# Optimization experiments

Measured on AMD Instinct MI355X. Metric: run time of the kernel, lower is better.

Reference implementation:

```python
import jax, jax.numpy as jnp
import numpy as np

B, T, M, PH, PW = 4, 8, 128, 48, 48
QD, CD, H, DH = 1024, 768, 8, 64
INNER = H * DH

def layer_norm(x, g, b, eps=1e-5):
    m = x.mean(-1, keepdims=True)
    v = ((x - m) ** 2).mean(-1, keepdims=True)
    return (x - m) * jax.lax.rsqrt(v + eps) * g + b

def setup_inputs():
    key = jax.random.key(0)
    ks = jax.random.split(key, 10)
    x = jax.random.normal(ks[0], (B * T, PH * PW, QD), jnp.float32)
    context = jax.random.normal(ks[1], (B, M, CD), jnp.float32)
    sg_node_positions = jax.random.normal(ks[2], (B, M, 3), jnp.float32) * 2.0
    # valid c2w: identity rotation + random translation (invertible)
    c2w = jnp.broadcast_to(jnp.eye(4, dtype=jnp.float32), (B, T, 4, 4))
    camera_c2w = c2w.at[..., :3, 3].set(jax.random.normal(ks[3], (B, T, 3), jnp.float32))
    intrinsics = jnp.broadcast_to(jnp.array([[1.0, 0.0, 0.5], [0.0, 1.0, 0.5], [0.0, 0.0, 1.0]], jnp.float32), (B, 3, 3))
    s = 0.02
    Wq = jax.random.normal(ks[4], (QD, INNER), jnp.float32) * s
    Wk = jax.random.normal(ks[5], (CD, INNER), jnp.float32) * s
    Wv = jax.random.normal(ks[6], (CD, INNER), jnp.float32) * s
    Wo = jax.random.normal(ks[7], (INNER, QD), jnp.float32) * s
    gate = jnp.array([0.1], jnp.float32)          # zero-init in module; nonzero so path is active
    spatial_gate = jnp.array([0.1], jnp.float32)
    spatial_log_sigma = jax.random.normal(ks[8], (H,), jnp.float32) * 0.1
    depth_log_alpha = jax.random.normal(ks[9], (H,), jnp.float32) * 0.1
    gamma_q = jnp.ones((QD,), jnp.float32); beta_q = jnp.zeros((QD,), jnp.float32)
    gamma_k = jnp.ones((CD,), jnp.float32); beta_k = jnp.zeros((CD,), jnp.float32)
    return dict(x=x, context=context, sg_node_positions=sg_node_positions, camera_c2w=camera_c2w,
                intrinsics=intrinsics, Wq=Wq, Wk=Wk, Wv=Wv, Wo=Wo, gate=gate, spatial_gate=spatial_gate,
                spatial_log_sigma=spatial_log_sigma, depth_log_alpha=depth_log_alpha,
                gamma_q=gamma_q, beta_q=beta_q, gamma_k=gamma_k, beta_k=beta_k,
                patch_h=PH, patch_w=PW)

def spatial_bias(sg_node_positions, camera_c2w, intrinsics, spatial_log_sigma, depth_log_alpha, patch_h, patch_w):
    Bb, Mn, _ = sg_node_positions.shape
    Tn = camera_c2w.shape[1]
    w2c = jnp.linalg.inv(camera_c2w)
    R = w2c[:, :, :3, :3]
    tv = w2c[:, :, :3, 3]
    p_cam = jnp.einsum('btij,bmj->btmi', R, sg_node_positions) + tv[:, :, None, :]  # (B,T,M,3)
    z = jnp.clip(p_cam[..., 2], 1e-4, None)
    fx = intrinsics[:, 0, 0]; fy = intrinsics[:, 1, 1]
    cx = intrinsics[:, 0, 2]; cy = intrinsics[:, 1, 2]
    u = fx[:, None, None] * (p_cam[..., 0] / z) + cx[:, None, None]   # (B,T,M)
    v = fy[:, None, None] * (p_cam[..., 1] / z) + cy[:, None, None]
    gy = (jnp.arange(patch_h, dtype=jnp.float32) + 0.5) / patch_h
    gx = (jnp.arange(patch_w, dtype=jnp.float32) + 0.5) / patch_w
    gyy, gxx = jnp.meshgrid(gy, gx, indexing='ij')
    gxx = gxx.reshape(-1); gyy = gyy.reshape(-1)                       # (P,)
    sq = (gxx[None, None, :, None] - u[:, :, None, :]) ** 2 + (gyy[None, None, :, None] - v[:, :, None, :]) ** 2  # (B,T,P,M)
    sigma = jnp.exp(spatial_log_sigma)
    inv2s = z[:, :, None, :] ** 2 / (2.0 * sigma[None, None, :, None] ** 2 + 1e-8)  # (B,T,H,M)
    bias = -sq[:, :, None, :, :] * inv2s[:, :, :, None, :]             # (B,T,H,P,M)
    depth_term = depth_log_alpha[None, None, :, None, None] * (-jnp.log(z))[:, :, None, None, :]
    bias = bias + depth_term
    behind = p_cam[..., 2] <= 0.0
    bias = jnp.where(behind[:, :, None, None, :], 0.0, bias)
    return bias.reshape(Bb * Tn, bias.shape[2], patch_h * patch_w, Mn)  # (BT,H,P,M)

def reference(x, context, sg_node_positions, camera_c2w, intrinsics, Wq, Wk, Wv, Wo, gate, spatial_gate,
              spatial_log_sigma, depth_log_alpha, gamma_q, beta_q, gamma_k, beta_k, patch_h, patch_w):
    BT, P, _ = x.shape
    Bb, Mn, _ = context.shape
    Tn = camera_c2w.shape[1]
    q = layer_norm(x, gamma_q, beta_q) @ Wq                            # (BT,P,INNER)
    ck = layer_norm(context, gamma_k, beta_k)
    k = ck @ Wk
    v = ck @ Wv
    q = q.reshape(BT, P, H, DH).transpose(0, 2, 1, 3)                  # (BT,H,P,DH)
    k = jnp.broadcast_to(k.reshape(Bb, 1, Mn, H, DH), (Bb, Tn, Mn, H, DH)).reshape(BT, Mn, H, DH).transpose(0, 2, 1, 3)
    v = jnp.broadcast_to(v.reshape(Bb, 1, Mn, H, DH), (Bb, Tn, Mn, H, DH)).reshape(BT, Mn, H, DH).transpose(0, 2, 1, 3)
    scores = jnp.einsum('bhpd,bhmd->bhpm', q, k) * (DH ** -0.5)        # (BT,H,P,M)
    bias = spatial_bias(sg_node_positions, camera_c2w, intrinsics, spatial_log_sigma, depth_log_alpha, patch_h, patch_w)
    scores = scores + jnp.tanh(spatial_gate) * bias
    attn = jax.nn.softmax(scores, axis=-1)
    out = jnp.einsum('bhpm,bhmd->bhpd', attn, v).transpose(0, 2, 1, 3).reshape(BT, P, INNER)
    return x + jnp.tanh(gate) * (out @ Wo)
```

## Files before the change

kernel.cpp:

```cpp
#include <hip/hip_runtime.h>
#include <hip/hip_bf16.h>
#include <stdint.h>
#include <cstddef>

typedef short short8 __attribute__((ext_vector_type(8)));
typedef float f32x4 __attribute__((ext_vector_type(4)));
typedef unsigned short us4 __attribute__((ext_vector_type(4)));
typedef unsigned short us8 __attribute__((ext_vector_type(8)));

#define DEV static __device__ __forceinline__

DEV unsigned short f2b(float f) {
  __hip_bfloat16 h = __float2bfloat16(f);
  return __builtin_bit_cast(unsigned short, h);
}

DEV void gload_lds16(const void* g, void* lds) {
  __builtin_amdgcn_global_load_lds((const __attribute__((address_space(1))) unsigned int*)g,
                                   (__attribute__((address_space(3))) unsigned int*)lds, 16, 0, 0);
}

__launch_bounds__(512, 2)
__global__ void gemm256(const unsigned short* __restrict__ A,
                        const unsigned short* __restrict__ Bt,
                        unsigned short* __restrict__ Cb,
                        int M, int N, int K)
{
  __shared__ __attribute__((aligned(16))) char lds[131072];
  const int tid  = threadIdx.x;
  const int lane = tid & 63, w = tid >> 6;
  const int wr = w >> 2, wc = w & 3;
  const int g = lane >> 4, lr = lane & 15;
  const int lrow  = lane >> 3;
  const int lslot = (lane & 7) ^ lrow;

  const int ntile = N >> 8;
  const int nwg = gridDim.x;
  const int bid = blockIdx.x;
  const int tile = ((nwg & 7) == 0) ? ((bid & 7)*(nwg >> 3) + (bid >> 3)) : bid;
  const size_t m0 = (size_t)(tile / ntile) << 8;
  const size_t n0 = (size_t)(tile % ntile) << 8;

  f32x4 acc[8][4] = {};

  auto STAGE = [&](int k0, int bufsel) {
    char* Ad = lds + bufsel*65536 + w*1024;
    char* Bd = Ad + 32768;
#pragma unroll
    for (int j = 0; j < 4; ++j) {
      const int row = j*64 + w*8 + lrow;
      gload_lds16(A  + (m0 + row)*(size_t)K + k0 + lslot*8, Ad + j*8192);
      gload_lds16(Bt + (n0 + row)*(size_t)K + k0 + lslot*8, Bd + j*8192);
    }
  };

  STAGE(0, 0);
  STAGE(64, 1);

  const int NT = K >> 6;
  for (int t = 0; t < NT; ++t) {
    const int cur = t & 1;
    if (t + 1 < NT) { asm volatile("s_waitcnt vmcnt(8)" ::: "memory"); }
    else            { asm volatile("s_waitcnt vmcnt(0)" ::: "memory"); }
    __builtin_amdgcn_s_barrier();
    __builtin_amdgcn_sched_barrier(0);

    const char* Ab = lds + cur*65536;
    const char* Bb = Ab + 32768;
#pragma unroll
    for (int ks = 0; ks < 2; ++ks) {
      short8 bfr[4];
#pragma unroll
      for (int nt = 0; nt < 4; ++nt) {
        const int row = wc*64 + nt*16 + lr;
        const int slot = (ks*4 + g) ^ (row & 7);
        bfr[nt] = *(const short8*)(Bb + row*128 + slot*16);
      }
#pragma unroll
      for (int mt = 0; mt < 8; ++mt) {
        const int row = wr*128 + mt*16 + lr;
        const int slot = (ks*4 + g) ^ (row & 7);
        short8 af = *(const short8*)(Ab + row*128 + slot*16);
#pragma unroll
        for (int nt = 0; nt < 4; ++nt)
          acc[mt][nt] = __builtin_amdgcn_mfma_f32_16x16x32_bf16(af, bfr[nt], acc[mt][nt], 0, 0, 0);
      }
    }

    __builtin_amdgcn_sched_barrier(0);
    __builtin_amdgcn_s_barrier();
    __builtin_amdgcn_sched_barrier(0);
    if (t + 2 < NT) STAGE((t + 2) << 6, cur);
  }

  float* Sw = (float*)(lds) + w*1024;
#pragma unroll
  for (int mt = 0; mt < 8; ++mt) {
#pragma unroll
    for (int nt = 0; nt < 4; ++nt)
#pragma unroll
      for (int r = 0; r < 4; ++r)
        Sw[(g*4 + r)*64 + nt*16 + lr] = acc[mt][nt][r];
#pragma unroll
    for (int rep = 0; rep < 2; ++rep) {
      const int row2 = rep*8 + (lane >> 3);
      const int colf = (lane & 7)*8;
      f32x4 a0 = *(const f32x4*)(Sw + row2*64 + colf);
      f32x4 a1 = *(const f32x4*)(Sw + row2*64 + colf + 4);
      us8 ov;
#pragma unroll
      for (int j = 0; j < 4; ++j) { ov[j] = f2b(a0[j]); ov[4+j] = f2b(a1[j]); }
      const size_t rowg = m0 + wr*128 + mt*16 + row2;
      *(us8*)(Cb + rowg * (size_t)N + (n0 + wc*64 + colf)) = ov;
    }
  }
}

template<int EPI>
__launch_bounds__(256, 2)
__global__ void gemm_bt(const unsigned short* __restrict__ A,
                        const unsigned short* __restrict__ Bt,
                        unsigned short* __restrict__ Cb,
                        float* __restrict__ Cf,
                        const float* __restrict__ xres,
                        const float* __restrict__ gatep,
                        int M, int N, int K)
{
  __shared__ __attribute__((aligned(16))) char As[16384];
  __shared__ __attribute__((aligned(16))) char Bs[16384];
  const int tid  = threadIdx.x;
  const int lane = tid & 63, w = tid >> 6;
  const int wr = w >> 1, wc = w & 1;
  const int g = lane >> 4, lr = lane & 15;
  const int ntile = N >> 7;
  const int nwg = gridDim.x;
  const int bid = blockIdx.x;
  const int tile = ((nwg & 7) == 0) ? ((bid & 7)*(nwg >> 3) + (bid >> 3)) : bid;
  const int m0 = (tile / ntile) << 7;
  const int n0 = (tile % ntile) << 7;

  const int lrow  = lane >> 3;
  const int lslot = (lane & 7) ^ lrow;

  f32x4 acc[4][4] = {};

  for (int k0 = 0; k0 < K; k0 += 64) {
#pragma unroll
    for (int c = 0; c < 4; ++c) {
      const int rowc = (w*4 + c)*8;
      gload_lds16(A  + (size_t)(m0 + rowc + lrow)*K + k0 + lslot*8, As + rowc*128);
      gload_lds16(Bt + (size_t)(n0 + rowc + lrow)*K + k0 + lslot*8, Bs + rowc*128);
    }
    __syncthreads();
#pragma unroll
    for (int ks = 0; ks < 2; ++ks) {
      short8 af[4], bfr[4];
#pragma unroll
      for (int mt = 0; mt < 4; ++mt) {
        int row = wr*64 + mt*16 + lr;
        int slot = (ks*4 + g) ^ (row & 7);
        af[mt] = *(const short8*)(As + row*128 + slot*16);
      }
#pragma unroll
      for (int nt = 0; nt < 4; ++nt) {
        int row = wc*64 + nt*16 + lr;
        int slot = (ks*4 + g) ^ (row & 7);
        bfr[nt] = *(const short8*)(Bs + row*128 + slot*16);
      }
#pragma unroll
      for (int mt = 0; mt < 4; ++mt)
#pragma unroll
        for (int nt = 0; nt < 4; ++nt)
          acc[mt][nt] = __builtin_amdgcn_mfma_f32_16x16x32_bf16(af[mt], bfr[nt], acc[mt][nt], 0, 0, 0);
    }
    __syncthreads();
  }

  float* Sw = (float*)(As) + w*1024;
  if (EPI == 1) {
    const float tg = tanhf(gatep[0]);
#pragma unroll
    for (int mt = 0; mt < 4; ++mt) {
#pragma unroll
      for (int nt = 0; nt < 4; ++nt)
#pragma unroll
        for (int r = 0; r < 4; ++r)
          Sw[(g*4 + r)*64 + nt*16 + lr] = acc[mt][nt][r];
#pragma unroll
      for (int rep = 0; rep < 4; ++rep) {
        int row2 = rep*4 + g;
        int colf = lr*4;
        f32x4 val = *(const f32x4*)(Sw + row2*64 + colf);
        size_t rowg = (size_t)(m0 + wr*64 + mt*16 + row2);
        size_t idx = rowg * (size_t)N + (n0 + wc*64 + colf);
        f32x4 xv = *(const f32x4*)(xres + idx);
#pragma unroll
        for (int j = 0; j < 4; ++j) val[j] = xv[j] + tg*val[j];
        *(f32x4*)(Cf + idx) = val;
      }
    }
  } else {
#pragma unroll
    for (int mt = 0; mt < 4; ++mt) {
#pragma unroll
      for (int nt = 0; nt < 4; ++nt)
#pragma unroll
        for (int r = 0; r < 4; ++r)
          Sw[(g*4 + r)*64 + nt*16 + lr] = acc[mt][nt][r];
#pragma unroll
      for (int rep = 0; rep < 2; ++rep) {
        int row2 = rep*8 + (lane >> 3);
        int colf = (lane & 7)*8;
        f32x4 a0 = *(const f32x4*)(Sw + row2*64 + colf);
        f32x4 a1 = *(const f32x4*)(Sw + row2*64 + colf + 4);
        us8 ov;
#pragma unroll
        for (int j = 0; j < 4; ++j) { ov[j] = f2b(a0[j]); ov[4+j] = f2b(a1[j]); }
        size_t rowg = (size_t)(m0 + wr*64 + mt*16 + row2);
        *(us8*)(Cb + rowg * (size_t)N + (n0 + wc*64 + colf)) = ov;
      }
    }
  }
}

__launch_bounds__(256, 2)
__global__ void gemm_kv(const unsigned short* __restrict__ ck,
                        const unsigned short* __restrict__ Wk_t,
                        const unsigned short* __restrict__ Wv_t,
                        unsigned short* __restrict__ Kb,
                        unsigned short* __restrict__ Vt)
{
  __shared__ __attribute__((aligned(16))) char As[16384];
  __shared__ __attribute__((aligned(16))) char Bs[16384];
  const int bid = blockIdx.x;
  const int kv = bid >> 4, bidl = bid & 15;
  const unsigned short* Bt = kv ? Wv_t : Wk_t;
  const int m0 = (bidl >> 2) << 7, n0 = (bidl & 3) << 7;
  const int tid  = threadIdx.x;
  const int lane = tid & 63, w = tid >> 6;
  const int wr = w >> 1, wc = w & 1;
  const int g = lane >> 4, lr = lane & 15;
  const int lrow  = lane >> 3;
  const int lslot = (lane & 7) ^ lrow;
  const int K = 768;

  f32x4 acc[4][4] = {};

  for (int k0 = 0; k0 < K; k0 += 64) {
#pragma unroll
    for (int c = 0; c < 4; ++c) {
      const int rowc = (w*4 + c)*8;
      gload_lds16(ck + (size_t)(m0 + rowc + lrow)*K + k0 + lslot*8, As + rowc*128);
      gload_lds16(Bt + (size_t)(n0 + rowc + lrow)*K + k0 + lslot*8, Bs + rowc*128);
    }
    __syncthreads();
#pragma unroll
    for (int ks = 0; ks < 2; ++ks) {
      short8 af[4], bfr[4];
#pragma unroll
      for (int mt = 0; mt < 4; ++mt) {
        int row = wr*64 + mt*16 + lr;
        int slot = (ks*4 + g) ^ (row & 7);
        af[mt] = *(const short8*)(As + row*128 + slot*16);
      }
#pragma unroll
      for (int nt = 0; nt < 4; ++nt) {
        int row = wc*64 + nt*16 + lr;
        int slot = (ks*4 + g) ^ (row & 7);
        bfr[nt] = *(const short8*)(Bs + row*128 + slot*16);
      }
#pragma unroll
      for (int mt = 0; mt < 4; ++mt)
#pragma unroll
        for (int nt = 0; nt < 4; ++nt)
          acc[mt][nt] = __builtin_amdgcn_mfma_f32_16x16x32_bf16(af[mt], bfr[nt], acc[mt][nt], 0, 0, 0);
    }
    __syncthreads();
  }

#pragma unroll
  for (int mt = 0; mt < 4; ++mt)
#pragma unroll
    for (int nt = 0; nt < 4; ++nt)
#pragma unroll
      for (int r = 0; r < 4; ++r) {
        int row = m0 + wr*64 + mt*16 + g*4 + r;
        int col = n0 + wc*64 + nt*16 + lr;
        int bb = row >> 7, mm = row & 127, hh = col >> 6, dd = col & 63;
        unsigned short val = f2b(acc[mt][nt][r]);
        if (kv == 0) Kb[(((size_t)(bb*8 + hh))*128 + mm)*64 + dd] = val;
        else         Vt[(((size_t)(bb*8 + hh))*64 + dd)*128 + mm] = val;
      }
}

template<int NSEG>
DEV void ln_rows_body(const float* __restrict__ in, const float* __restrict__ gamma,
                      const float* __restrict__ beta, unsigned short* __restrict__ out,
                      int C, int blk, int tid)
{
  const int lane = tid & 63;
  const size_t row = (size_t)blk*4 + (tid >> 6);
  const float* rp = in + row * (size_t)C;
  f32x4 vals[NSEG];
  float s = 0.f, sq = 0.f;
#pragma unroll
  for (int i = 0; i < NSEG; ++i) {
    f32x4 v = *(const f32x4*)(rp + (i*64 + lane)*4);
    vals[i] = v;
#pragma unroll
    for (int j = 0; j < 4; ++j) { s += v[j]; sq += v[j]*v[j]; }
  }
#pragma unroll
  for (int off = 32; off >= 1; off >>= 1) {
    s  += __shfl_xor(s, off);
    sq += __shfl_xor(sq, off);
  }
  const float invC = 1.0f / (float)C;
  float mean = s * invC;
  float var  = sq * invC - mean*mean;
  float rstd = rsqrtf(var + 1e-5f);
#pragma unroll
  for (int i = 0; i < NSEG; ++i) {
    int cb = (i*64 + lane)*4;
    f32x4 gm = *(const f32x4*)(gamma + cb);
    f32x4 bb = *(const f32x4*)(beta + cb);
    us4 ov;
#pragma unroll
    for (int j = 0; j < 4; ++j)
      ov[j] = f2b((vals[i][j] - mean)*rstd*gm[j] + bb[j]);
    *(us4*)(out + row * (size_t)C + cb) = ov;
  }
}

__global__ void ln_big(const float* __restrict__ in, const float* __restrict__ gamma,
                       const float* __restrict__ beta, unsigned short* __restrict__ out)
{
  ln_rows_body<4>(in, gamma, beta, out, 1024, blockIdx.x, threadIdx.x);
}

__global__ void prep(const float* __restrict__ Wq, const float* __restrict__ Wk,
                     const float* __restrict__ Wv, const float* __restrict__ Wo,
                     unsigned short* __restrict__ Wq_t, unsigned short* __restrict__ Wk_t,
                     unsigned short* __restrict__ Wv_t, unsigned short* __restrict__ Wo_t,
                     const float* __restrict__ ctx, const float* __restrict__ gk,
                     const float* __restrict__ bk, unsigned short* __restrict__ ck,
                     const float* __restrict__ pos, const float* __restrict__ c2w,
                     const float* __restrict__ intr, const float* __restrict__ sls,
                     const float* __restrict__ dla,
                     float* __restrict__ u_o, float* __restrict__ v_o, float* __restrict__ bh_o,
                     float* __restrict__ iv_o, float* __restrict__ dp_o)
{
  __shared__ float tile[32][33];
  int bidx = blockIdx.x;
  if (bidx < 1792) {
    const float* src; unsigned short* dst; int R, C;
    if (bidx < 512)       { src = Wq; dst = Wq_t; R = 1024; C = 512; }
    else if (bidx < 896)  { src = Wk; dst = Wk_t; R = 768;  C = 512;  bidx -= 512; }
    else if (bidx < 1280) { src = Wv; dst = Wv_t; R = 768;  C = 512;  bidx -= 896; }
    else                  { src = Wo; dst = Wo_t; R = 512;  C = 1024; bidx -= 1280; }
    const int cb = C >> 5;
    const int bx = bidx % cb, by = bidx / cb;
    const int tx = threadIdx.x & 31, ty = threadIdx.x >> 5;
#pragma unroll
    for (int i = 0; i < 32; i += 8)
      tile[ty + i][tx] = src[(size_t)(by*32 + ty + i)*C + bx*32 + tx];
    __syncthreads();
#pragma unroll
    for (int i = 0; i < 32; i += 8)
      dst[(size_t)(bx*32 + ty + i)*R + by*32 + tx] = f2b(tile[tx][ty + i]);
    return;
  }
  if (bidx < 1920) {
    ln_rows_body<3>(ctx, gk, bk, ck, 768, bidx - 1792, threadIdx.x);
    return;
  }
  if (threadIdx.x >= 128) return;
  const int bt = bidx - 1920;
  const int b = bt >> 3;
  const int m = threadIdx.x;
  const float* Mc = c2w + (size_t)bt*16;
  float r00=Mc[0], r01=Mc[1], r02=Mc[2],  t0=Mc[3];
  float r10=Mc[4], r11=Mc[5], r12=Mc[6],  t1=Mc[7];
  float r20=Mc[8], r21=Mc[9], r22=Mc[10], t2=Mc[11];
  float a00 = r11*r22 - r12*r21;
  float a01 = r02*r21 - r01*r22;
  float a02 = r01*r12 - r02*r11;
  float a10 = r12*r20 - r10*r22;
  float a11 = r00*r22 - r02*r20;
  float a12 = r02*r10 - r00*r12;
  float a20 = r10*r21 - r11*r20;
  float a21 = r01*r20 - r00*r21;
  float a22 = r00*r11 - r01*r10;
  float det = r00*a00 + r01*a10 + r02*a20;
  float id = 1.0f/det;
  a00*=id; a01*=id; a02*=id; a10*=id; a11*=id; a12*=id; a20*=id; a21*=id; a22*=id;
  float tv0 = -(a00*t0 + a01*t1 + a02*t2);
  float tv1 = -(a10*t0 + a11*t1 + a12*t2);
  float tv2 = -(a20*t0 + a21*t1 + a22*t2);
  const float* pm = pos + (size_t)(b*128 + m)*3;
  float px = pm[0], py = pm[1], pz = pm[2];
  float x = a00*px + a01*py + a02*pz + tv0;
  float y = a10*px + a11*py + a12*pz + tv1;
  float zraw = a20*px + a21*py + a22*pz + tv2;
  float z = fmaxf(zraw, 1e-4f);
  float fx = intr[b*9 + 0], fy = intr[b*9 + 4], cx = intr[b*9 + 2], cy = intr[b*9 + 5];
  u_o[bt*128 + m] = fx*(x/z) + cx;
  v_o[bt*128 + m] = fy*(y/z) + cy;
  bh_o[bt*128 + m] = (zraw <= 0.0f) ? 1.0f : 0.0f;
  float lz = __logf(z);
#pragma unroll
  for (int hh = 0; hh < 8; ++hh) {
    float sg = __expf(sls[hh]);
    iv_o[(size_t)(bt*8 + hh)*128 + m] = z*z / (2.0f*sg*sg + 1e-8f);
    dp_o[(size_t)(bt*8 + hh)*128 + m] = dla[hh] * (-lz);
  }
}

__launch_bounds__(256, 2)
__global__ void attn_kernel(const unsigned short* __restrict__ q,
                            const unsigned short* __restrict__ Kb,
                            const unsigned short* __restrict__ Vt,
                            const float* __restrict__ ub, const float* __restrict__ vb,
                            const float* __restrict__ bhb,
                            const float* __restrict__ ivb, const float* __restrict__ dpb,
                            const float* __restrict__ sgate,
                            unsigned short* __restrict__ out)
{
  const int bid = blockIdx.x;
  const int ptile = bid % 18;
  const int h  = (bid / 18) & 7;
  const int bt = bid / (18*8);
  const int b  = bt >> 3;
  const int lane = threadIdx.x & 63, w = threadIdx.x >> 6;
  const int g = lane >> 4, lr = lane & 15;
  const int p0 = ptile*128 + w*32;

  const float sg = tanhf(sgate[0]);
  const unsigned short* Kh = Kb + ((size_t)(b*8 + h)) * (128*64);
  const unsigned short* Vh = Vt + ((size_t)(b*8 + h)) * (64*128);
  const unsigned short* qh = q + (size_t)bt*2304*512 + h*64;

  short8 qf[2][2];
#pragma unroll
  for (int pt = 0; pt < 2; ++pt)
#pragma unroll
    for (int ks = 0; ks < 2; ++ks)
      qf[pt][ks] = *(const short8*)(qh + (size_t)(p0 + pt*16 + lr)*512 + ks*32 + g*8);

  f32x4 st[8][2] = {};
#pragma unroll
  for (int mt = 0; mt < 8; ++mt) {
#pragma unroll
    for (int ks = 0; ks < 2; ++ks) {
      short8 kf = *(const short8*)(Kh + (mt*16 + lr)*64 + ks*32 + g*8);
#pragma unroll
      for (int pt = 0; pt < 2; ++pt)
        st[mt][pt] = __builtin_amdgcn_mfma_f32_16x16x32_bf16(kf, qf[pt][ks], st[mt][pt], 0, 0, 0);
    }
  }

  float gx[2], gy[2];
#pragma unroll
  for (int pt = 0; pt < 2; ++pt) {
    int p = p0 + pt*16 + lr;
    int py = p / 48, px = p - py*48;
    gx[pt] = (px + 0.5f) * (1.0f/48.0f);
    gy[pt] = (py + 0.5f) * (1.0f/48.0f);
  }
  const float* uB = ub  + bt*128;
  const float* vB = vb  + bt*128;
  const float* bB = bhb + bt*128;
  const float* iB = ivb + (size_t)(bt*8 + h)*128;
  const float* dB = dpb + (size_t)(bt*8 + h)*128;

  float pmax[2] = {-3.0e38f, -3.0e38f};
#pragma unroll
  for (int mt = 0; mt < 8; ++mt) {
    int mb = mt*16 + g*4;
    f32x4 uu = *(const f32x4*)(uB + mb);
    f32x4 vv = *(const f32x4*)(vB + mb);
    f32x4 bh = *(const f32x4*)(bB + mb);
    f32x4 iv = *(const f32x4*)(iB + mb);
    f32x4 dp = *(const f32x4*)(dB + mb);
#pragma unroll
    for (int r = 0; r < 4; ++r) {
#pragma unroll
      for (int pt = 0; pt < 2; ++pt) {
        float du = gx[pt] - uu[r], dv = gy[pt] - vv[r];
        float bias = (bh[r] != 0.0f) ? 0.0f : (-(du*du + dv*dv)*iv[r] + dp[r]);
        float s = st[mt][pt][r]*0.125f + sg*bias;
        st[mt][pt][r] = s;
        pmax[pt] = fmaxf(pmax[pt], s);
      }
    }
  }
#pragma unroll
  for (int pt = 0; pt < 2; ++pt) {
    pmax[pt] = fmaxf(pmax[pt], __shfl_xor(pmax[pt], 16));
    pmax[pt] = fmaxf(pmax[pt], __shfl_xor(pmax[pt], 32));
  }
  float psum[2] = {0.f, 0.f};
#pragma unroll
  for (int mt = 0; mt < 8; ++mt)
#pragma unroll
    for (int pt = 0; pt < 2; ++pt)
#pragma unroll
      for (int r = 0; r < 4; ++r) {
        float e = __expf(st[mt][pt][r] - pmax[pt]);
        st[mt][pt][r] = e;
        psum[pt] += e;
      }
#pragma unroll
  for (int pt = 0; pt < 2; ++pt) {
    psum[pt] += __shfl_xor(psum[pt], 16);
    psum[pt] += __shfl_xor(psum[pt], 32);
  }
  float pinv[2] = {1.0f/psum[0], 1.0f/psum[1]};

  short8 pf[2][4];
#pragma unroll
  for (int pt = 0; pt < 2; ++pt)
#pragma unroll
    for (int ms = 0; ms < 4; ++ms)
#pragma unroll
      for (int i = 0; i < 8; ++i)
        pf[pt][ms][i] = (short)f2b(st[ms*2 + (i>>2)][pt][i & 3] * pinv[pt]);

  f32x4 o[4][2] = {};
#pragma unroll
  for (int ms = 0; ms < 4; ++ms) {
#pragma unroll
    for (int dt = 0; dt < 4; ++dt) {
      const unsigned short* vp = Vh + (size_t)(dt*16 + lr)*128 + ms*32 + g*4;
      us4 v0 = *(const us4*)(vp);
      us4 v1 = *(const us4*)(vp + 16);
      short8 vf;
#pragma unroll
      for (int i = 0; i < 4; ++i) { vf[i] = (short)v0[i]; vf[i+4] = (short)v1[i]; }
#pragma unroll
      for (int pt = 0; pt < 2; ++pt)
        o[dt][pt] = __builtin_amdgcn_mfma_f32_16x16x32_bf16(vf, pf[pt][ms], o[dt][pt], 0, 0, 0);
    }
  }

#pragma unroll
  for (int dt = 0; dt < 4; ++dt)
#pragma unroll
    for (int pt = 0; pt < 2; ++pt) {
      int p = p0 + pt*16 + lr;
      int d = h*64 + dt*16 + g*4;
      us4 ov;
#pragma unroll
      for (int r = 0; r < 4; ++r) ov[r] = f2b(o[dt][pt][r]);
      *(us4*)(out + (size_t)(bt*2304 + p)*512 + d) = ov;
    }
}

extern "C" void kernel_launch(void* const* d_in, const int* in_sizes, int n_in,
                              void* d_out, int out_size, void* d_ws, size_t ws_size,
                              hipStream_t stream)
{
  const float* x     = (const float*)d_in[0];
  const float* ctx   = (const float*)d_in[1];
  const float* pos   = (const float*)d_in[2];
  const float* c2w   = (const float*)d_in[3];
  const float* intr  = (const float*)d_in[4];
  const float* Wq    = (const float*)d_in[5];
  const float* Wk    = (const float*)d_in[6];
  const float* Wv    = (const float*)d_in[7];
  const float* Wo    = (const float*)d_in[8];
  const float* gate  = (const float*)d_in[9];
  const float* sgate = (const float*)d_in[10];
  const float* sls   = (const float*)d_in[11];
  const float* dla   = (const float*)d_in[12];
  const float* gq    = (const float*)d_in[13];
  const float* bq    = (const float*)d_in[14];
  const float* gk    = (const float*)d_in[15];
  const float* bk    = (const float*)d_in[16];

  char* ws = (char*)d_ws;
  size_t off = 0;
  auto alloc = [&](size_t bytes) {
    char* p = ws + off;
    off += (bytes + 255) & ~(size_t)255;
    return p;
  };
  unsigned short* ln_x  = (unsigned short*)alloc(73728ull*1024*2);
  unsigned short* qbuf  = (unsigned short*)alloc(73728ull*512*2);
  unsigned short* Wq_t  = (unsigned short*)alloc(512ull*1024*2);
  unsigned short* Wk_t  = (unsigned short*)alloc(512ull*768*2);
  unsigned short* Wv_t  = (unsigned short*)alloc(512ull*768*2);
  unsigned short* Wo_t  = (unsigned short*)alloc(1024ull*512*2);
  unsigned short* ck    = (unsigned short*)alloc(512ull*768*2);
  unsigned short* Kbuf  = (unsigned short*)alloc(4ull*8*128*64*2);
  unsigned short* Vtb   = (unsigned short*)alloc(4ull*8*64*128*2);
  float* u_o  = (float*)alloc(32*128*4);
  float* v_o  = (float*)alloc(32*128*4);
  float* bh_o = (float*)alloc(32*128*4);
  float* iv_o = (float*)alloc(32ull*8*128*4);
  float* dp_o = (float*)alloc(32ull*8*128*4);
  unsigned short* attn_out = ln_x;

  prep<<<1952, 256, 0, stream>>>(Wq, Wk, Wv, Wo, Wq_t, Wk_t, Wv_t, Wo_t,
                                 ctx, gk, bk, ck,
                                 pos, c2w, intr, sls, dla,
                                 u_o, v_o, bh_o, iv_o, dp_o);

  ln_big<<<73728/4, 256, 0, stream>>>(x, gq, bq, ln_x);

  gemm_kv<<<32, 256, 0, stream>>>(ck, Wk_t, Wv_t, Kbuf, Vtb);

  gemm256<<<(73728/256)*(512/256), 512, 0, stream>>>(ln_x, Wq_t, qbuf, 73728, 512, 1024);

  attn_kernel<<<32*8*18, 256, 0, stream>>>(qbuf, Kbuf, Vtb, u_o, v_o, bh_o, iv_o, dp_o, sgate, attn_out);

  gemm_bt<1><<<(73728/128)*(1024/128), 256, 0, stream>>>(attn_out, Wo_t, nullptr, (float*)d_out, x, gate, 73728, 1024, 512);
}
```

Before: 510.9 us.

## Restructure Q-projection GEMM into 8-phase pipelined schedule with split half-tile loads

Rewrites the 256x256 Q-projection GEMM main loop into an eight-phase schedule that processes two K-tiles per iteration. Each phase loads a quarter of the register fragments from LDS, issues one half-tile global-to-LDS load, and runs a 4x2 MFMA quadrant between barriers. s_setprio is raised around the MFMAs. The goal is to interleave global loads, LDS reads and MFMA work more finely so memory latency is hidden. The cost is many more barriers per K-step and more complex vmcnt bookkeeping.

```diff
diff --git a/kernel.cpp b/kernel.cpp
--- a/kernel.cpp
+++ b/kernel.cpp
@@ -21,19 +21,16 @@
 }
 
 __launch_bounds__(512, 2)
-__global__ void gemm256(const unsigned short* __restrict__ A,
-                        const unsigned short* __restrict__ Bt,
-                        unsigned short* __restrict__ Cb,
-                        int M, int N, int K)
+__global__ void gemm256_8ph(const unsigned short* __restrict__ A,
+                            const unsigned short* __restrict__ Bt,
+                            unsigned short* __restrict__ Cb,
+                            int M, int N, int K)
 {
   __shared__ __attribute__((aligned(16))) char lds[131072];
-  const int tid  = threadIdx.x;
+  const int tid = threadIdx.x;
   const int lane = tid & 63, w = tid >> 6;
   const int wr = w >> 2, wc = w & 3;
   const int g = lane >> 4, lr = lane & 15;
-  const int lrow  = lane >> 3;
-  const int lslot = (lane & 7) ^ lrow;
-
   const int ntile = N >> 8;
   const int nwg = gridDim.x;
   const int bid = blockIdx.x;
@@ -41,58 +38,135 @@
   const size_t m0 = (size_t)(tile / ntile) << 8;
   const size_t n0 = (size_t)(tile % ntile) << 8;
 
+  const int srl = tid >> 3;
+  const int sgc = ((tid & 7) ^ (srl & 7)) * 8;
+
+#define STAGEH(X, grow0, k0, ldsoff)                                           \
+  do {                                                                         \
+    char* hb_ = lds + (ldsoff) + w*1024;                                       \
+    gload_lds16((X) + ((grow0) + srl)*(size_t)K + (k0) + sgc, hb_);            \
+    gload_lds16((X) + ((grow0) + 64 + srl)*(size_t)K + (k0) + sgc, hb_ + 8192);\
+  } while (0)
+
+#define BAR() do { __builtin_amdgcn_sched_barrier(0); __builtin_amdgcn_s_barrier(); __builtin_amdgcn_sched_barrier(0); } while (0)
+
   f32x4 acc[8][4] = {};
-
-  auto STAGE = [&](int k0, int bufsel) {
-    char* Ad = lds + bufsel*65536 + w*1024;
-    char* Bd = Ad + 32768;
-#pragma unroll
-    for (int j = 0; j < 4; ++j) {
-      const int row = j*64 + w*8 + lrow;
-      gload_lds16(A  + (m0 + row)*(size_t)K + k0 + lslot*8, Ad + j*8192);
-      gload_lds16(Bt + (n0 + row)*(size_t)K + k0 + lslot*8, Bd + j*8192);
-    }
-  };
-
-  STAGE(0, 0);
-  STAGE(64, 1);
-
-  const int NT = K >> 6;
-  for (int t = 0; t < NT; ++t) {
-    const int cur = t & 1;
-    if (t + 1 < NT) { asm volatile("s_waitcnt vmcnt(8)" ::: "memory"); }
-    else            { asm volatile("s_waitcnt vmcnt(0)" ::: "memory"); }
-    __builtin_amdgcn_s_barrier();
-    __builtin_amdgcn_sched_barrier(0);
-
-    const char* Ab = lds + cur*65536;
-    const char* Bb = Ab + 32768;
-#pragma unroll
-    for (int ks = 0; ks < 2; ++ks) {
-      short8 bfr[4];
-#pragma unroll
-      for (int nt = 0; nt < 4; ++nt) {
-        const int row = wc*64 + nt*16 + lr;
-        const int slot = (ks*4 + g) ^ (row & 7);
-        bfr[nt] = *(const short8*)(Bb + row*128 + slot*16);
-      }
-#pragma unroll
-      for (int mt = 0; mt < 8; ++mt) {
-        const int row = wr*128 + mt*16 + lr;
-        const int slot = (ks*4 + g) ^ (row & 7);
-        short8 af = *(const short8*)(Ab + row*128 + slot*16);
-#pragma unroll
-        for (int nt = 0; nt < 4; ++nt)
-          acc[mt][nt] = __builtin_amdgcn_mfma_f32_16x16x32_bf16(af, bfr[nt], acc[mt][nt], 0, 0, 0);
-      }
-    }
-
-    __builtin_amdgcn_sched_barrier(0);
-    __builtin_amdgcn_s_barrier();
-    __builtin_amdgcn_sched_barrier(0);
-    if (t + 2 < NT) STAGE((t + 2) << 6, cur);
-  }
-
+  short8 aF[4][2], bF[4][2];
+
+  int aoff[2], boff[2];
+#pragma unroll
+  for (int kk = 0; kk < 2; ++kk) {
+    const int sl = (((kk*4 + g) ^ (lr & 7)) * 16);
+    aoff[kk] = wr*16384 + lr*128 + sl;
+    boff[kk] = 32768 + (wc >> 1)*16384 + ((wc & 1)*64 + lr)*128 + sl;
+  }
+
+#define MFQ(mh, nh)                                                            \
+  do {                                                                         \
+    __builtin_amdgcn_s_setprio(1);                                             \
+    _Pragma("unroll")                                                          \
+    for (int kk = 0; kk < 2; ++kk)                                             \
+      _Pragma("unroll")                                                        \
+      for (int mt = 0; mt < 4; ++mt)                                           \
+        _Pragma("unroll")                                                      \
+        for (int nt = 0; nt < 2; ++nt)                                         \
+          acc[(mh)*4+mt][(nh)*2+nt] = __builtin_amdgcn_mfma_f32_16x16x32_bf16( \
+              aF[mt][kk], bF[(nh)*2+nt][kk], acc[(mh)*4+mt][(nh)*2+nt], 0,0,0);\
+    __builtin_amdgcn_s_setprio(0);                                             \
+  } while (0)
+
+  STAGEH(A,  m0,       0, 0);
+  STAGEH(A,  m0 + 128, 0, 16384);
+  STAGEH(Bt, n0,       0, 32768);
+  STAGEH(Bt, n0 + 128, 0, 49152);
+  STAGEH(Bt, n0,       64, 65536 + 32768);
+  STAGEH(Bt, n0 + 128, 64, 65536 + 49152);
+  asm volatile("s_waitcnt vmcnt(4)" ::: "memory");
+  __builtin_amdgcn_s_barrier();
+
+  const int NI = K >> 7;
+  for (int i = 0; i < NI; ++i) {
+    const int T = 2*i;
+    const bool nl = (i + 1 < NI);
+    const int kA1 = (T + 1) << 6;
+    const int kT2 = (T + 2) << 6;
+    const int kT3 = (T + 3) << 6;
+
+#pragma unroll
+    for (int kk = 0; kk < 2; ++kk) {
+#pragma unroll
+      for (int mt = 0; mt < 4; ++mt) aF[mt][kk] = *(const short8*)(lds + mt*2048 + aoff[kk]);
+#pragma unroll
+      for (int nf = 0; nf < 2; ++nf) bF[nf][kk] = *(const short8*)(lds + nf*2048 + boff[kk]);
+    }
+    STAGEH(A, m0, kA1, 65536);
+    BAR();
+    MFQ(0, 0);
+    BAR();
+#pragma unroll
+    for (int kk = 0; kk < 2; ++kk)
+#pragma unroll
+      for (int nf = 2; nf < 4; ++nf) bF[nf][kk] = *(const short8*)(lds + nf*2048 + boff[kk]);
+    STAGEH(A, m0 + 128, kA1, 65536 + 16384);
+    BAR();
+    MFQ(0, 1);
+    BAR();
+#pragma unroll
+    for (int kk = 0; kk < 2; ++kk)
+#pragma unroll
+      for (int mt = 0; mt < 4; ++mt) aF[mt][kk] = *(const short8*)(lds + (4+mt)*2048 + aoff[kk]);
+    if (nl) STAGEH(Bt, n0, kT2, 32768);
+    BAR();
+    MFQ(1, 0);
+    BAR();
+    if (nl) {
+      STAGEH(Bt, n0 + 128, kT2, 49152);
+      asm volatile("s_waitcnt vmcnt(4)" ::: "memory");
+    } else {
+      asm volatile("s_waitcnt vmcnt(0)" ::: "memory");
+    }
+    BAR();
+    MFQ(1, 1);
+    BAR();
+
+#pragma unroll
+    for (int kk = 0; kk < 2; ++kk) {
+#pragma unroll
+      for (int mt = 0; mt < 4; ++mt) aF[mt][kk] = *(const short8*)(lds + 65536 + mt*2048 + aoff[kk]);
+#pragma unroll
+      for (int nf = 0; nf < 2; ++nf) bF[nf][kk] = *(const short8*)(lds + 65536 + nf*2048 + boff[kk]);
+    }
+    if (nl) STAGEH(A, m0, kT2, 0);
+    BAR();
+    MFQ(0, 0);
+    BAR();
+#pragma unroll
+    for (int kk = 0; kk < 2; ++kk)
+#pragma unroll
+      for (int nf = 2; nf < 4; ++nf) bF[nf][kk] = *(const short8*)(lds + 65536 + nf*2048 + boff[kk]);
+    if (nl) STAGEH(A, m0 + 128, kT2, 16384);
+    BAR();
+    MFQ(0, 1);
+    BAR();
+#pragma unroll
+    for (int kk = 0; kk < 2; ++kk)
+#pragma unroll
+      for (int mt = 0; mt < 4; ++mt) aF[mt][kk] = *(const short8*)(lds + 65536 + (4+mt)*2048 + aoff[kk]);
+    if (nl) STAGEH(Bt, n0, kT3, 65536 + 32768);
+    BAR();
+    MFQ(1, 0);
+    BAR();
+    if (nl) {
+      STAGEH(Bt, n0 + 128, kT3, 65536 + 49152);
+      asm volatile("s_waitcnt vmcnt(4)" ::: "memory");
+    }
+    BAR();
+    MFQ(1, 1);
+    BAR();
+  }
+
+  asm volatile("s_waitcnt vmcnt(0)" ::: "memory");
+  __builtin_amdgcn_s_barrier();
   float* Sw = (float*)(lds) + w*1024;
 #pragma unroll
   for (int mt = 0; mt < 8; ++mt) {
@@ -114,6 +188,9 @@
       *(us8*)(Cb + rowg * (size_t)N + (n0 + wc*64 + colf)) = ov;
     }
   }
+#undef STAGEH
+#undef BAR
+#undef MFQ
 }
 
 template<int EPI>
@@ -610,7 +687,7 @@
 
   gemm_kv<<<32, 256, 0, stream>>>(ck, Wk_t, Wv_t, Kbuf, Vtb);
 
-  gemm256<<<(73728/256)*(512/256), 512, 0, stream>>>(ln_x, Wq_t, qbuf, 73728, 512, 1024);
+  gemm256_8ph<<<(73728/256)*(512/256), 512, 0, stream>>>(ln_x, Wq_t, qbuf, 73728, 512, 1024);
 
   attn_kernel<<<32*8*18, 256, 0, stream>>>(qbuf, Kbuf, Vtb, u_o, v_o, bh_o, iv_o, dp_o, sgate, attn_out);
 
```

After: 494.6 us (median of 3 runs). 3.2% less time.
